# Kernel tuning notes

Measured on AMD Instinct MI355X. Metric: run time of the kernel, lower is better.

Reference implementation:

```python
import jax, jax.numpy as jnp
import numpy as np

N = 500000
D = 128
B = 16384

def setup_inputs() -> dict:
    key = jax.random.key(0)
    k1, k2, k3, k4 = jax.random.split(key, 4)
    x = jax.random.normal(k1, (N, D), dtype=jnp.float32)
    ref = jax.random.normal(k2, (N, D), dtype=jnp.float32)
    index = jnp.sort(jax.random.randint(k3, (N,), 0, B))
    W = jax.random.normal(k4, (2 * D, 1), dtype=jnp.float32) * (1.0 / np.sqrt(2 * D))
    b = jnp.zeros((1,), dtype=jnp.float32)
    return {"x": x, "ref": ref, "index": index, "batch_size": B, "W": W, "b": b}

def reference(x, ref, index, batch_size, W, b):
    # src: [N, 1] attention logits
    src = jnp.tanh(jnp.concatenate([x, ref], axis=-1) @ W + b)
    # segment softmax (max is detached in the original via .detach())
    seg_max = jax.ops.segment_max(jax.lax.stop_gradient(src), index,
                                  num_segments=batch_size)
    out = jnp.exp(src - seg_max[index])
    out_sum = jax.ops.segment_sum(out, index, num_segments=batch_size) + 1e-16
    w = out / out_sum[index]            # [N, 1] normalized weights
    # weighted sum of x per segment -> [batch_size, D]
    return jax.ops.segment_sum(w * x, index, num_segments=batch_size)
```

## Files before the change

### kernel.cpp

```cpp
#include <hip/hip_runtime.h>
#include <math.h>

#define D 128

__global__ __launch_bounds__(256) void seg_starts_kernel(
    const int* __restrict__ index, int* __restrict__ starts, int N, int B)
{
    int i = blockIdx.x * blockDim.x + threadIdx.x;
    if (i >= N) return;
    int cur  = index[i];
    int prev = (i == 0) ? -1 : index[i - 1];
    for (int j = prev + 1; j <= cur; ++j) starts[j] = i;
    if (i == N - 1) {
        for (int j = cur + 1; j <= B; ++j) starts[j] = N;
    }
}

__device__ __forceinline__ float fast_exp_tanh(float v) {
    float e2 = __expf(2.0f * v);
    float th = 1.0f - 2.0f * __builtin_amdgcn_rcpf(1.0f + e2);
    return __expf(th);
}

__global__ __launch_bounds__(256) void attn_seg_kernel(
    const float* __restrict__ x,
    const float* __restrict__ ref,
    const int*   __restrict__ starts,
    const float* __restrict__ W,
    const float* __restrict__ b,
    float*       __restrict__ out)
{
    const int seg  = blockIdx.x;
    const int tid  = threadIdx.x;
    const int wave = tid >> 6;
    const int lane = tid & 63;
    const int hl   = lane >> 5;
    const int c    = lane & 31;

    const int start = starts[seg];
    const int end   = starts[seg + 1];
    const int cnt   = end - start;

    const float4 wx = ((const float4*)W)[c];
    const float4 wr = ((const float4*)(W + D))[c];
    const float bias = b[0];

    float4 acc   = make_float4(0.f, 0.f, 0.f, 0.f);
    float  sum_e = 0.f;

    const int niter = (cnt + 7) >> 3;
    const int rbase = start + (wave << 1) + hl;

    if (niter > 0) {
        const int last = end - 1;
        int cur_r = rbase;
        int row   = min(cur_r, last);
        float4 xv = ((const float4*)(x   + (size_t)row * D))[c];
        float4 rv = ((const float4*)(ref + (size_t)row * D))[c];

        for (int it = 1; it < niter; ++it) {
            const int nxt_r = rbase + (it << 3);
            const int nrow  = min(nxt_r, last);
            float4 xn = ((const float4*)(x   + (size_t)nrow * D))[c];
            float4 rn = ((const float4*)(ref + (size_t)nrow * D))[c];

            float partial = xv.x*wx.x + xv.y*wx.y + xv.z*wx.z + xv.w*wx.w
                          + rv.x*wr.x + rv.y*wr.y + rv.z*wr.z + rv.w*wr.w;
            #pragma unroll
            for (int off = 16; off >= 1; off >>= 1)
                partial += __shfl_xor(partial, off);
            float e = fast_exp_tanh(partial + bias);
            e = (cur_r < end) ? e : 0.f;
            acc.x += e * xv.x; acc.y += e * xv.y;
            acc.z += e * xv.z; acc.w += e * xv.w;
            sum_e += e;

            xv = xn; rv = rn; cur_r = nxt_r;
        }

        float partial = xv.x*wx.x + xv.y*wx.y + xv.z*wx.z + xv.w*wx.w
                      + rv.x*wr.x + rv.y*wr.y + rv.z*wr.z + rv.w*wr.w;
        #pragma unroll
        for (int off = 16; off >= 1; off >>= 1)
            partial += __shfl_xor(partial, off);
        float e = fast_exp_tanh(partial + bias);
        e = (cur_r < end) ? e : 0.f;
        acc.x += e * xv.x; acc.y += e * xv.y;
        acc.z += e * xv.z; acc.w += e * xv.w;
        sum_e += e;
    }

    __shared__ float lds_acc[8][D];
    __shared__ float lds_sum[8];
    const int half_id = (wave << 1) | hl;
    ((float4*)lds_acc[half_id])[c] = acc;
    if (c == 0) lds_sum[half_id] = sum_e;
    __syncthreads();

    if (tid < D) {
        float t = 0.f;
        float s = 1e-16f;
        #pragma unroll
        for (int k = 0; k < 8; ++k) t += lds_acc[k][tid];
        #pragma unroll
        for (int k = 0; k < 8; ++k) s += lds_sum[k];
        out[(size_t)seg * D + tid] = t / s;
    }
}

extern "C" void kernel_launch(void* const* d_in, const int* in_sizes, int n_in,
                              void* d_out, int out_size, void* d_ws, size_t ws_size,
                              hipStream_t stream) {
    const float* x     = (const float*)d_in[0];
    const float* ref   = (const float*)d_in[1];
    const int*   index = (const int*)d_in[2];
    const float* W     = (const float*)d_in[4];
    const float* b     = (const float*)d_in[5];
    float* out = (float*)d_out;

    const int N = in_sizes[0] / D;
    const int B = out_size / D;

    int* starts = (int*)d_ws;

    seg_starts_kernel<<<(N + 255) / 256, 256, 0, stream>>>(index, starts, N, B);
    attn_seg_kernel<<<B, 256, 0, stream>>>(x, ref, starts, W, b, out);
}
```

Measured before the change: 496.2 us.

## Map one wavefront per segment with double-buffered row prefetch

Reassigns work so each 64-lane wave processes a whole segment instead of a 256-thread block per segment, packing four segments per block. Each wave processes two rows per step while prefetching the next two, and the final half-wave combine uses a lane shuffle instead of LDS plus a block barrier. This removes shared-memory traffic, the sync, and idle waves on short segments. The trade-off is less parallelism per segment, so long segments take longer.

Measured after the change: 503.6 us. About the same (+1.5%).

```diff
diff --git a/kernel.cpp b/kernel.cpp
--- a/kernel.cpp
+++ b/kernel.cpp
@@ -22,18 +22,36 @@
     return __expf(th);
 }
 
+__device__ __forceinline__ void seg_step(
+    const float4& xv, const float4& rv, int r, int end,
+    const float4& wx, const float4& wr, float bias,
+    float4& acc, float& sum_e)
+{
+    float partial = xv.x*wx.x + xv.y*wx.y + xv.z*wx.z + xv.w*wx.w
+                  + rv.x*wr.x + rv.y*wr.y + rv.z*wr.z + rv.w*wr.w;
+    #pragma unroll
+    for (int off = 16; off >= 1; off >>= 1)
+        partial += __shfl_xor(partial, off);
+    float e = fast_exp_tanh(partial + bias);
+    e = (r < end) ? e : 0.f;
+    acc.x += e * xv.x; acc.y += e * xv.y;
+    acc.z += e * xv.z; acc.w += e * xv.w;
+    sum_e += e;
+}
+
 __global__ __launch_bounds__(256) void attn_seg_kernel(
     const float* __restrict__ x,
     const float* __restrict__ ref,
     const int*   __restrict__ starts,
     const float* __restrict__ W,
     const float* __restrict__ b,
-    float*       __restrict__ out)
+    float*       __restrict__ out,
+    int B)
 {
-    const int seg  = blockIdx.x;
-    const int tid  = threadIdx.x;
-    const int wave = tid >> 6;
-    const int lane = tid & 63;
+    const int wave = threadIdx.x >> 6;
+    const int seg  = blockIdx.x * 4 + wave;
+    if (seg >= B) return;
+    const int lane = threadIdx.x & 63;
     const int hl   = lane >> 5;
     const int c    = lane & 31;
 
@@ -48,63 +66,51 @@
     float4 acc   = make_float4(0.f, 0.f, 0.f, 0.f);
     float  sum_e = 0.f;
 
-    const int niter = (cnt + 7) >> 3;
-    const int rbase = start + (wave << 1) + hl;
+    if (cnt > 0) {
+        const int last  = end - 1;
+        const int niter = (cnt + 1) >> 1;
 
-    if (niter > 0) {
-        const int last = end - 1;
-        int cur_r = rbase;
-        int row   = min(cur_r, last);
-        float4 xv = ((const float4*)(x   + (size_t)row * D))[c];
-        float4 rv = ((const float4*)(ref + (size_t)row * D))[c];
+        int r0 = start + hl;
+        int p0 = min(r0, last);
+        float4 xa = ((const float4*)(x   + (size_t)p0 * D))[c];
+        float4 fa = ((const float4*)(ref + (size_t)p0 * D))[c];
+        int r1 = r0 + 2;
+        int p1 = min(r1, last);
+        float4 xb = ((const float4*)(x   + (size_t)p1 * D))[c];
+        float4 fb = ((const float4*)(ref + (size_t)p1 * D))[c];
 
-        for (int it = 1; it < niter; ++it) {
-            const int nxt_r = rbase + (it << 3);
-            const int nrow  = min(nxt_r, last);
-            float4 xn = ((const float4*)(x   + (size_t)nrow * D))[c];
-            float4 rn = ((const float4*)(ref + (size_t)nrow * D))[c];
+        int t = 0;
+        for (; t + 2 < niter; t += 2) {
+            const int r2 = r0 + 4; const int p2 = min(r2, last);
+            float4 xc = ((const float4*)(x   + (size_t)p2 * D))[c];
+            float4 fc = ((const float4*)(ref + (size_t)p2 * D))[c];
+            const int r3 = r1 + 4; const int p3 = min(r3, last);
+            float4 xd = ((const float4*)(x   + (size_t)p3 * D))[c];
+            float4 fd = ((const float4*)(ref + (size_t)p3 * D))[c];
 
-            float partial = xv.x*wx.x + xv.y*wx.y + xv.z*wx.z + xv.w*wx.w
-                          + rv.x*wr.x + rv.y*wr.y + rv.z*wr.z + rv.w*wr.w;
-            #pragma unroll
-            for (int off = 16; off >= 1; off >>= 1)
-                partial += __shfl_xor(partial, off);
-            float e = fast_exp_tanh(partial + bias);
-            e = (cur_r < end) ? e : 0.f;
-            acc.x += e * xv.x; acc.y += e * xv.y;
-            acc.z += e * xv.z; acc.w += e * xv.w;
-            sum_e += e;
+            seg_step(xa, fa, r0, end, wx, wr, bias, acc, sum_e);
+            seg_step(xb, fb, r1, end, wx, wr, bias, acc, sum_e);
 
-            xv = xn; rv = rn; cur_r = nxt_r;
+            xa = xc; fa = fc; r0 = r2;
+            xb = xd; fb = fd; r1 = r3;
         }
-
-        float partial = xv.x*wx.x + xv.y*wx.y + xv.z*wx.z + xv.w*wx.w
-                      + rv.x*wr.x + rv.y*wr.y + rv.z*wr.z + rv.w*wr.w;
-        #pragma unroll
-        for (int off = 16; off >= 1; off >>= 1)
-            partial += __shfl_xor(partial, off);
-        float e = fast_exp_tanh(partial + bias);
-        e = (cur_r < end) ? e : 0.f;
-        acc.x += e * xv.x; acc.y += e * xv.y;
-        acc.z += e * xv.z; acc.w += e * xv.w;
-        sum_e += e;
+        seg_step(xa, fa, r0, end, wx, wr, bias, acc, sum_e);
+        if (t + 1 < niter)
+            seg_step(xb, fb, r1, end, wx, wr, bias, acc, sum_e);
     }
 
-    __shared__ float lds_acc[8][D];
-    __shared__ float lds_sum[8];
-    const int half_id = (wave << 1) | hl;
-    ((float4*)lds_acc[half_id])[c] = acc;
-    if (c == 0) lds_sum[half_id] = sum_e;
-    __syncthreads();
+    acc.x += __shfl_xor(acc.x, 32);
+    acc.y += __shfl_xor(acc.y, 32);
+    acc.z += __shfl_xor(acc.z, 32);
+    acc.w += __shfl_xor(acc.w, 32);
+    sum_e += __shfl_xor(sum_e, 32);
 
-    if (tid < D) {
-        float t = 0.f;
-        float s = 1e-16f;
-        #pragma unroll
-        for (int k = 0; k < 8; ++k) t += lds_acc[k][tid];
-        #pragma unroll
-        for (int k = 0; k < 8; ++k) s += lds_sum[k];
-        out[(size_t)seg * D + tid] = t / s;
+    if (hl == 0) {
+        const float inv = 1.0f / (sum_e + 1e-16f);
+        float4 o;
+        o.x = acc.x * inv; o.y = acc.y * inv;
+        o.z = acc.z * inv; o.w = acc.w * inv;
+        ((float4*)(out + (size_t)seg * D))[c] = o;
     }
 }
 
@@ -124,5 +130,5 @@
     int* starts = (int*)d_ws;
 
     seg_starts_kernel<<<(N + 255) / 256, 256, 0, stream>>>(index, starts, N, B);
-    attn_seg_kernel<<<B, 256, 0, stream>>>(x, ref, starts, W, b, out);
+    attn_seg_kernel<<<(B + 3) / 4, 256, 0, stream>>>(x, ref, starts, W, b, out, B);
 }
```
